# Performance work log

Hardware: AMD Instinct MI355X
Metric: run time of the kernel (lower is better)

## Reference

```python
import jax, jax.numpy as jnp
import numpy as np

B, CIN, H, W = 16, 1, 256, 256
WIDTH = 64
MODES = 32
LAYERS = 4
COUT = 1


def conv1x1(x, w, b):
    # x: [B,Ci,H,W], w: [Co,Ci], b: [Co]
    return jnp.einsum('bixy,oi->boxy', x, w) + b[None, :, None, None]


def mlp(x, w1, b1, w2, b2):
    # Conv2d(ci,mid,1) -> GELU(exact) -> Conv2d(mid,co,1)
    return conv1x1(jax.nn.gelu(conv1x1(x, w1, b1), approximate=False), w2, b2)


def spectral_conv2d(x, w1r, w1i, w2r, w2i):
    # x: [B,C,H,W]; weights: [Ci,Co,m1,m2] (real/imag parts of cfloat params)
    b, c, h, w = x.shape
    m1, m2 = w1r.shape[2], w1r.shape[3]
    co = w1r.shape[1]
    x_ft = jnp.fft.rfft2(x)  # [B,C,H,W//2+1] complex64
    w1 = w1r + 1j * w1i
    w2 = w2r + 1j * w2i
    top = jnp.einsum('bixy,ioxy->boxy', x_ft[:, :, :m1, :m2], w1)
    bot = jnp.einsum('bixy,ioxy->boxy', x_ft[:, :, -m1:, :m2], w2)
    out_ft = jnp.zeros((b, co, h, w // 2 + 1), dtype=x_ft.dtype)
    out_ft = out_ft.at[:, :, :m1, :m2].set(top).at[:, :, -m1:, :m2].set(bot)
    return jnp.fft.irfft2(out_ft, s=(h, w))


def setup_inputs() -> dict:
    key = jax.random.key(0)
    ks = iter(jax.random.split(key, 32))
    scale = 1.0 / (WIDTH * WIDTH)
    f32 = jnp.float32
    inp = {}
    inp['x'] = jax.random.normal(next(ks), (B, CIN, H, W), dtype=f32)
    # lifting 1x1 conv
    inp['p_w'] = jax.random.normal(next(ks), (WIDTH, CIN), dtype=f32) / np.sqrt(CIN)
    inp['p_b'] = jnp.zeros((WIDTH,), dtype=f32)
    # per-layer spectral weights (real/imag of uniform cfloat init)
    shp = (LAYERS, WIDTH, WIDTH, MODES, MODES)
    inp['sw1r'] = scale * jax.random.uniform(next(ks), shp, dtype=f32)
    inp['sw1i'] = scale * jax.random.uniform(next(ks), shp, dtype=f32)
    inp['sw2r'] = scale * jax.random.uniform(next(ks), shp, dtype=f32)
    inp['sw2i'] = scale * jax.random.uniform(next(ks), shp, dtype=f32)
    # per-layer channel MLP (mid_channels = WIDTH)
    inp['m1w'] = jax.random.normal(next(ks), (LAYERS, WIDTH, WIDTH), dtype=f32) / np.sqrt(WIDTH)
    inp['m1b'] = jnp.zeros((LAYERS, WIDTH), dtype=f32)
    inp['m2w'] = jax.random.normal(next(ks), (LAYERS, WIDTH, WIDTH), dtype=f32) / np.sqrt(WIDTH)
    inp['m2b'] = jnp.zeros((LAYERS, WIDTH), dtype=f32)
    # per-layer skip 1x1 conv
    inp['skw'] = jax.random.normal(next(ks), (LAYERS, WIDTH, WIDTH), dtype=f32) / np.sqrt(WIDTH)
    inp['skb'] = jnp.zeros((LAYERS, WIDTH), dtype=f32)
    # projection MLP (mid = 4*WIDTH)
    inp['q1w'] = jax.random.normal(next(ks), (4 * WIDTH, WIDTH), dtype=f32) / np.sqrt(WIDTH)
    inp['q1b'] = jnp.zeros((4 * WIDTH,), dtype=f32)
    inp['q2w'] = jax.random.normal(next(ks), (COUT, 4 * WIDTH), dtype=f32) / np.sqrt(4 * WIDTH)
    inp['q2b'] = jnp.zeros((COUT,), dtype=f32)
    return inp


def reference(x, p_w, p_b, sw1r, sw1i, sw2r, sw2i, m1w, m1b, m2w, m2b,
              skw, skb, q1w, q1b, q2w, q2b):
    h = conv1x1(x, p_w, p_b)  # lift to [B,WIDTH,H,W]
    for l in range(LAYERS):
        x1 = spectral_conv2d(h, sw1r[l], sw1i[l], sw2r[l], sw2i[l])
        x1 = mlp(x1, m1w[l], m1b[l], m2w[l], m2b[l])
        x2 = conv1x1(h, skw[l], skb[l])
        h = x1 + x2
        if l < LAYERS - 1:
            h = jax.nn.gelu(h, approximate=False)
    return mlp(h, q1w, q1b, q2w, q2b)  # [B,COUT,H,W]
```

## Files before the change

kernel.cpp:

```cpp
#include <hip/hip_runtime.h>
#include <math.h>

#define NC 64
#define NH 256
#define NW 256
#define NM 32
#define NKY 64
#define HW 65536

typedef short bfrag __attribute__((ext_vector_type(8)));
typedef float facc  __attribute__((ext_vector_type(4)));
#define MFMA(a,b,c) __builtin_amdgcn_mfma_f32_16x16x32_bf16(a,b,c,0,0,0)

static constexpr float PI_F = 3.14159265358979323846f;

__device__ __forceinline__ unsigned short f2b(float f) {
  unsigned b = __float_as_uint(f);
  return (unsigned short)((b + 0x7FFFu + ((b >> 16) & 1u)) >> 16);
}
__device__ __forceinline__ float b2f(unsigned short h) {
  return __uint_as_float((unsigned)h << 16);
}

__device__ __forceinline__ float gelu_f(float x) {
  float z = fabsf(x) * 0.70710678118654752f;
  float t = 1.0f / (1.0f + 0.3275911f * z);
  float e = __expf(-z * z);
  float p = t * (0.254829592f + t * (-0.284496736f + t * (1.421413741f +
            t * (-1.453152027f + t * 1.061405429f))));
  float er = copysignf(1.0f - p * e, x);
  return 0.5f * x * (1.0f + er);
}

__global__ void k_tEy(unsigned short* __restrict__ eh, unsigned short* __restrict__ el) {
  int i = blockIdx.x * 256 + threadIdx.x;
  int m = i >> 8, y = i & 255;
  int kyi = m & 63;
  int ky = (kyi < 32) ? kyi : (192 + kyi);
  int a = (ky * y) & 255;
  float s, c; sincosf((float)a * (PI_F / 128.f), &s, &c);
  float v = (m < 64) ? c : -s;
  unsigned short h = f2b(v);
  eh[i] = h; el[i] = f2b(v - b2f(h));
}
__global__ void k_tEx(unsigned short* __restrict__ eh, unsigned short* __restrict__ el) {
  int i = blockIdx.x * 256 + threadIdx.x;
  int m = i >> 9, k = i & 511;
  int x = k & 255, plane = k >> 8, kx = m & 31;
  int a = (kx * x) & 255;
  float s, c; sincosf((float)a * (PI_F / 128.f), &s, &c);
  float v = (m < 32) ? (plane ? s : c) : (plane ? c : -s);
  unsigned short h = f2b(v);
  eh[i] = h; el[i] = f2b(v - b2f(h));
}
__global__ void k_tWy(unsigned short* __restrict__ eh, unsigned short* __restrict__ el) {
  int i = blockIdx.x * 256 + threadIdx.x;
  int row = i >> 7, k = i & 127;
  int y = row & 255, part = row >> 8;
  int kyi = k & 63, plane = k >> 6;
  int ky = (kyi < 32) ? kyi : (192 + kyi);
  int a = (ky * y) & 255;
  float s, c; sincosf((float)a * (PI_F / 128.f), &s, &c);
  float v = (part == 0) ? (plane ? -s : c) : (plane ? c : s);
  unsigned short h = f2b(v);
  eh[i] = h; el[i] = f2b(v - b2f(h));
}
__global__ void k_tCx(unsigned short* __restrict__ eh, unsigned short* __restrict__ el) {
  int i = blockIdx.x * 256 + threadIdx.x;
  int x = i >> 6, k = i & 63;
  int kx = k & 31, plane = k >> 5;
  float w = ((kx == 0) ? 1.0f : 2.0f) / 65536.0f;
  int a = (kx * x) & 255;
  float s, c; sincosf((float)a * (PI_F / 128.f), &s, &c);
  float v = plane ? (-w * s) : (w * c);
  unsigned short h = f2b(v);
  eh[i] = h; el[i] = f2b(v - b2f(h));
}

__global__ void k_cvt2(const float* __restrict__ src, unsigned short* __restrict__ hi,
                       unsigned short* __restrict__ lo, int n) {
  int i = blockIdx.x * 256 + threadIdx.x;
  if (i < n) {
    float v = src[i];
    unsigned short h = f2b(v);
    hi[i] = h;
    lo[i] = f2b(v - b2f(h));
  }
}

__global__ __launch_bounds__(256) void k_lift(const float* __restrict__ x,
                                              const float* __restrict__ pw,
                                              const float* __restrict__ pb,
                                              float* __restrict__ h) {
  int b = blockIdx.y;
  int yx = blockIdx.x * 256 + threadIdx.x;
  float v = x[(size_t)b * HW + yx];
  float* hp = h + (size_t)b * NC * HW + yx;
  for (int c = 0; c < NC; ++c) hp[(size_t)c * HW] = v * pw[c] + pb[c];
}

__global__ __launch_bounds__(256) void k_fy2(const float* __restrict__ h,
                                             const unsigned short* __restrict__ Ah,
                                             const unsigned short* __restrict__ Al,
                                             float* __restrict__ Xc, int Ncol) {
  int tid = threadIdx.x, wv = tid >> 6, ln = tid & 63, g16 = ln >> 4, l15 = ln & 15;
  int colbase = blockIdx.x * 128 + wv * 32;
  facc acc[8][2];
#pragma unroll
  for (int mf = 0; mf < 8; ++mf)
#pragma unroll
    for (int pf = 0; pf < 2; ++pf) acc[mf][pf] = (facc)0.f;
#pragma unroll 1
  for (int ks = 0; ks < 8; ++ks) {
    int kof = g16 * 8 + 32 * ks;
    bfrag bh[2], bl[2];
#pragma unroll
    for (int pf = 0; pf < 2; ++pf) {
      int col = colbase + pf * 16 + l15;
      const float* hp = h + (size_t)(col >> 8) * HW + (col & 255) + (size_t)kof * 256;
#pragma unroll
      for (int j = 0; j < 8; ++j) {
        float v = hp[j * 256];
        unsigned short hi = f2b(v);
        bh[pf][j] = (short)hi;
        bl[pf][j] = (short)f2b(v - b2f(hi));
      }
    }
#pragma unroll
    for (int mf = 0; mf < 8; ++mf) {
      int row = 16 * mf + l15;
      bfrag ah = *(const bfrag*)(Ah + row * 256 + kof);
      bfrag al = *(const bfrag*)(Al + row * 256 + kof);
#pragma unroll
      for (int pf = 0; pf < 2; ++pf) {
        acc[mf][pf] = MFMA(ah, bh[pf], acc[mf][pf]);
        acc[mf][pf] = MFMA(ah, bl[pf], acc[mf][pf]);
        acc[mf][pf] = MFMA(al, bh[pf], acc[mf][pf]);
      }
    }
  }
#pragma unroll
  for (int mf = 0; mf < 8; ++mf)
#pragma unroll
    for (int pf = 0; pf < 2; ++pf) {
      int col = colbase + pf * 16 + l15;
#pragma unroll
      for (int r = 0; r < 4; ++r)
        Xc[(size_t)(16 * mf + 4 * g16 + r) * Ncol + col] = acc[mf][pf][r];
    }
}

__global__ __launch_bounds__(256) void k_fx2(const float* __restrict__ Xc,
                                             const unsigned short* __restrict__ Ah,
                                             const unsigned short* __restrict__ Al,
                                             float* __restrict__ X2r,
                                             float* __restrict__ X2i, int NcXc) {
  int tid = threadIdx.x, wv = tid >> 6, ln = tid & 63, g16 = ln >> 4, l15 = ln & 15;
  int colbase = blockIdx.x * 128 + wv * 32;
  facc acc[4][2];
#pragma unroll
  for (int mf = 0; mf < 4; ++mf)
#pragma unroll
    for (int pf = 0; pf < 2; ++pf) acc[mf][pf] = (facc)0.f;
#pragma unroll 1
  for (int ks = 0; ks < 16; ++ks) {
    int plane = ks >> 3;
    int x0 = (ks & 7) * 32 + g16 * 8;
    int kof = g16 * 8 + 32 * ks;
    bfrag bh[2], bl[2];
#pragma unroll
    for (int pf = 0; pf < 2; ++pf) {
      int col = colbase + pf * 16 + l15;
      const float* p = Xc + (size_t)(plane * 64 + (col & 63)) * NcXc + (col >> 6) * 256 + x0;
      float4 u0 = *(const float4*)p;
      float4 u1 = *(const float4*)(p + 4);
      float tv[8] = {u0.x, u0.y, u0.z, u0.w, u1.x, u1.y, u1.z, u1.w};
#pragma unroll
      for (int j = 0; j < 8; ++j) {
        unsigned short hi = f2b(tv[j]);
        bh[pf][j] = (short)hi;
        bl[pf][j] = (short)f2b(tv[j] - b2f(hi));
      }
    }
#pragma unroll
    for (int mf = 0; mf < 4; ++mf) {
      int row = 16 * mf + l15;
      bfrag ah = *(const bfrag*)(Ah + row * 512 + kof);
      bfrag al = *(const bfrag*)(Al + row * 512 + kof);
#pragma unroll
      for (int pf = 0; pf < 2; ++pf) {
        acc[mf][pf] = MFMA(ah, bh[pf], acc[mf][pf]);
        acc[mf][pf] = MFMA(ah, bl[pf], acc[mf][pf]);
        acc[mf][pf] = MFMA(al, bh[pf], acc[mf][pf]);
      }
    }
  }
#pragma unroll
  for (int mf = 0; mf < 4; ++mf)
#pragma unroll
    for (int pf = 0; pf < 2; ++pf) {
      int col = colbase + pf * 16 + l15;
      float* base = (mf >= 2) ? X2i : X2r;
      int kxb = 16 * (mf & 1) + 4 * g16;
      float4 v = make_float4(acc[mf][pf][0], acc[mf][pf][1], acc[mf][pf][2], acc[mf][pf][3]);
      *(float4*)(base + (size_t)col * 32 + kxb) = v;
    }
}

__global__ __launch_bounds__(512) void k_spec(const float* __restrict__ X2r,
                                              const float* __restrict__ X2i,
                                              const float* __restrict__ w1r,
                                              const float* __restrict__ w1i,
                                              const float* __restrict__ w2r,
                                              const float* __restrict__ w2i,
                                              float* __restrict__ S, int Ncs) {
  int b = blockIdx.y;
  int och = blockIdx.x & 3;
  int kyi = blockIdx.x >> 2;
  __shared__ float2 xs[NC * NM];
  for (int idx = threadIdx.x; idx < NC * NM; idx += 512) {
    int i = idx >> 5, kx = idx & 31;
    size_t c2 = ((size_t)(b * 64 + i) * 64 + kyi) * 32 + kx;
    xs[idx] = make_float2(X2r[c2], X2i[c2]);
  }
  __syncthreads();
  int kx = threadIdx.x & 31;
  int ol = threadIdx.x >> 5;
  int o = och * 16 + ol;
  int kym = kyi & 31;
  const float* wr = (kyi < 32) ? w1r : w2r;
  const float* wi = (kyi < 32) ? w1i : w2i;
  size_t wb = ((size_t)o * NM + kym) * NM + kx;
  float ar = 0.f, ai = 0.f;
#pragma unroll 4
  for (int i = 0; i < NC; ++i) {
    float2 xv = xs[i * NM + kx];
    float wrv = wr[wb + (size_t)i * 65536];
    float wiv = wi[wb + (size_t)i * 65536];
    ar += xv.x * wrv - xv.y * wiv;
    ai += xv.x * wiv + xv.y * wrv;
  }
  size_t cco = (size_t)(b * 64 + o) * 32 + kx;
  S[(size_t)kyi * Ncs + cco] = ar;
  S[(size_t)(64 + kyi) * Ncs + cco] = ai;
}

__global__ __launch_bounds__(256) void k_iy2(const float* __restrict__ S,
                                             const unsigned short* __restrict__ Ah,
                                             const unsigned short* __restrict__ Al,
                                             float* __restrict__ t2, int Ncs) {
  int tid = threadIdx.x, wv = tid >> 6, ln = tid & 63, g16 = ln >> 4, l15 = ln & 15;
  int colbase = blockIdx.x * 128 + wv * 32;
  int rowb = blockIdx.y * 64;
  facc acc[4][2];
#pragma unroll
  for (int mf = 0; mf < 4; ++mf)
#pragma unroll
    for (int pf = 0; pf < 2; ++pf) acc[mf][pf] = (facc)0.f;
#pragma unroll 1
  for (int ks = 0; ks < 4; ++ks) {
    int kof = g16 * 8 + 32 * ks;
    bfrag bh[2], bl[2];
#pragma unroll
    for (int pf = 0; pf < 2; ++pf) {
      int col = colbase + pf * 16 + l15;
      const float* p = S + (size_t)kof * Ncs + col;
#pragma unroll
      for (int j = 0; j < 8; ++j) {
        float v = p[(size_t)j * Ncs];
        unsigned short hi = f2b(v);
        bh[pf][j] = (short)hi;
        bl[pf][j] = (short)f2b(v - b2f(hi));
      }
    }
#pragma unroll
    for (int mf = 0; mf < 4; ++mf) {
      int row = rowb + 16 * mf + l15;
      bfrag ah = *(const bfrag*)(Ah + row * 128 + kof);
      bfrag al = *(const bfrag*)(Al + row * 128 + kof);
#pragma unroll
      for (int pf = 0; pf < 2; ++pf) {
        acc[mf][pf] = MFMA(ah, bh[pf], acc[mf][pf]);
        acc[mf][pf] = MFMA(ah, bl[pf], acc[mf][pf]);
        acc[mf][pf] = MFMA(al, bh[pf], acc[mf][pf]);
      }
    }
  }
#pragma unroll
  for (int mf = 0; mf < 4; ++mf)
#pragma unroll
    for (int pf = 0; pf < 2; ++pf) {
      int col = colbase + pf * 16 + l15;
#pragma unroll
      for (int r = 0; r < 4; ++r)
        t2[(size_t)(rowb + 16 * mf + 4 * g16 + r) * Ncs + col] = acc[mf][pf][r];
    }
}

__global__ __launch_bounds__(256) void k_ix2(const float* __restrict__ t2,
                                             const unsigned short* __restrict__ Ah,
                                             const unsigned short* __restrict__ Al,
                                             unsigned short* __restrict__ x1h,
                                             unsigned short* __restrict__ x1l, int Nct) {
  int tid = threadIdx.x, wv = tid >> 6, ln = tid & 63, g16 = ln >> 4, l15 = ln & 15;
  int colbase = blockIdx.x * 128 + wv * 32;
  int rowb = blockIdx.y * 128;
  facc acc[8][2];
#pragma unroll
  for (int mf = 0; mf < 8; ++mf)
#pragma unroll
    for (int pf = 0; pf < 2; ++pf) acc[mf][pf] = (facc)0.f;
#pragma unroll 1
  for (int ks = 0; ks < 2; ++ks) {
    int kof = g16 * 8 + 32 * ks;
    bfrag bh[2], bl[2];
#pragma unroll
    for (int pf = 0; pf < 2; ++pf) {
      int col = colbase + pf * 16 + l15;
      const float* p = t2 + (size_t)(ks * 256 + (col & 255)) * Nct + (col >> 8) * 32 + g16 * 8;
      float4 u0 = *(const float4*)p;
      float4 u1 = *(const float4*)(p + 4);
      float tv[8] = {u0.x, u0.y, u0.z, u0.w, u1.x, u1.y, u1.z, u1.w};
#pragma unroll
      for (int j = 0; j < 8; ++j) {
        unsigned short hi = f2b(tv[j]);
        bh[pf][j] = (short)hi;
        bl[pf][j] = (short)f2b(tv[j] - b2f(hi));
      }
    }
#pragma unroll
    for (int mf = 0; mf < 8; ++mf) {
      int row = rowb + 16 * mf + l15;
      bfrag ah = *(const bfrag*)(Ah + row * 64 + kof);
      bfrag al = *(const bfrag*)(Al + row * 64 + kof);
#pragma unroll
      for (int pf = 0; pf < 2; ++pf) {
        acc[mf][pf] = MFMA(ah, bh[pf], acc[mf][pf]);
        acc[mf][pf] = MFMA(ah, bl[pf], acc[mf][pf]);
        acc[mf][pf] = MFMA(al, bh[pf], acc[mf][pf]);
      }
    }
  }
#pragma unroll
  for (int mf = 0; mf < 8; ++mf)
#pragma unroll
    for (int pf = 0; pf < 2; ++pf) {
      int col = colbase + pf * 16 + l15;
      int bc = col >> 8, y = col & 255;
      int xb = rowb + 16 * mf + 4 * g16;
      ushort4 hv, lv;
#pragma unroll
      for (int r = 0; r < 4; ++r) {
        float v = acc[mf][pf][r];
        unsigned short hi = f2b(v);
        ((unsigned short*)&hv)[r] = hi;
        ((unsigned short*)&lv)[r] = f2b(v - b2f(hi));
      }
      size_t o = (size_t)bc * HW + y * 256 + xb;
      *(ushort4*)(x1h + o) = hv;
      *(ushort4*)(x1l + o) = lv;
    }
}

__global__ __launch_bounds__(256) void k_mlp1s(unsigned short* __restrict__ x1h,
                                               unsigned short* __restrict__ x1l,
                                               const unsigned short* __restrict__ w1h,
                                               const unsigned short* __restrict__ w1l,
                                               const float* __restrict__ b1p) {
  __shared__ unsigned short whs[64 * 72], wls[64 * 72];
  int tid = threadIdx.x;
  for (int i = tid; i < 64 * 64; i += 256) {
    int r = i >> 6, c = i & 63;
    whs[r * 72 + c] = w1h[i];
    wls[r * 72 + c] = w1l[i];
  }
  int wv = tid >> 6, ln = tid & 63, g16 = ln >> 4, l15 = ln & 15;
  int b = blockIdx.y;
  unsigned short* xh = x1h + (size_t)b * NC * HW;
  unsigned short* xl = x1l + (size_t)b * NC * HW;
  float b1v[4][4];
#pragma unroll
  for (int mf = 0; mf < 4; ++mf)
#pragma unroll
    for (int r = 0; r < 4; ++r) b1v[mf][r] = b1p[16 * mf + 4 * g16 + r];
  __syncthreads();
  for (int t = 0; t < 4; ++t) {
    int pxb = (blockIdx.x * 4 + t) * 128 + wv * 32;
    facc a1[4][2];
#pragma unroll
    for (int mf = 0; mf < 4; ++mf)
#pragma unroll
      for (int pf = 0; pf < 2; ++pf) {
        facc z; z[0] = b1v[mf][0]; z[1] = b1v[mf][1]; z[2] = b1v[mf][2]; z[3] = b1v[mf][3];
        a1[mf][pf] = z;
      }
#pragma unroll
    for (int ks = 0; ks < 2; ++ks) {
      bfrag xhb[2], xlb[2];
#pragma unroll
      for (int pf = 0; pf < 2; ++pf) {
        int px = pxb + pf * 16 + l15;
#pragma unroll
        for (int j = 0; j < 8; ++j) {
          int c = g16 * 8 + j + 32 * ks;
          xhb[pf][j] = (short)xh[(size_t)c * HW + px];
          xlb[pf][j] = (short)xl[(size_t)c * HW + px];
        }
      }
#pragma unroll
      for (int mf = 0; mf < 4; ++mf) {
        bfrag wh = *(const bfrag*)(whs + (16 * mf + l15) * 72 + g16 * 8 + 32 * ks);
        bfrag wl = *(const bfrag*)(wls + (16 * mf + l15) * 72 + g16 * 8 + 32 * ks);
#pragma unroll
        for (int pf = 0; pf < 2; ++pf) {
          a1[mf][pf] = MFMA(wh, xhb[pf], a1[mf][pf]);
          a1[mf][pf] = MFMA(wh, xlb[pf], a1[mf][pf]);
          a1[mf][pf] = MFMA(wl, xhb[pf], a1[mf][pf]);
        }
      }
    }
#pragma unroll
    for (int mf = 0; mf < 4; ++mf)
#pragma unroll
      for (int pf = 0; pf < 2; ++pf) {
        int px = pxb + pf * 16 + l15;
#pragma unroll
        for (int r = 0; r < 4; ++r) {
          float v = gelu_f(a1[mf][pf][r]);
          unsigned short hi = f2b(v);
          size_t idx = (size_t)(16 * mf + 4 * g16 + r) * HW + px;
          xh[idx] = hi;
          xl[idx] = f2b(v - b2f(hi));
        }
      }
  }
}

__global__ __launch_bounds__(256) void k_mix2(const unsigned short* __restrict__ midh,
                                              const unsigned short* __restrict__ midl,
                                              float* __restrict__ h,
                                              const unsigned short* __restrict__ w2h,
                                              const unsigned short* __restrict__ w2l,
                                              const unsigned short* __restrict__ skh,
                                              const unsigned short* __restrict__ skl,
                                              const float* __restrict__ b2p,
                                              const float* __restrict__ skbp,
                                              int do_gelu) {
  __shared__ unsigned short w2hs[64 * 72], w2ls[64 * 72], skhs[64 * 72], skls[64 * 72];
  int tid = threadIdx.x;
  for (int i = tid; i < 64 * 64; i += 256) {
    int r = i >> 6, c = i & 63;
    w2hs[r * 72 + c] = w2h[i];
    w2ls[r * 72 + c] = w2l[i];
    skhs[r * 72 + c] = skh[i];
    skls[r * 72 + c] = skl[i];
  }
  int wv = tid >> 6, ln = tid & 63, g16 = ln >> 4, l15 = ln & 15;
  int b = blockIdx.y;
  const unsigned short* mh = midh + (size_t)b * NC * HW;
  const unsigned short* ml = midl + (size_t)b * NC * HW;
  float* hb = h + (size_t)b * NC * HW;
  float b2v[4][4];
#pragma unroll
  for (int mf = 0; mf < 4; ++mf)
#pragma unroll
    for (int r = 0; r < 4; ++r) {
      int o = 16 * mf + 4 * g16 + r;
      b2v[mf][r] = b2p[o] + skbp[o];
    }
  __syncthreads();
  for (int t = 0; t < 4; ++t) {
    int pxb = (blockIdx.x * 4 + t) * 128 + wv * 32;
    facc a2[4][2];
#pragma unroll
    for (int mf = 0; mf < 4; ++mf)
#pragma unroll
      for (int pf = 0; pf < 2; ++pf) {
        facc z; z[0] = b2v[mf][0]; z[1] = b2v[mf][1]; z[2] = b2v[mf][2]; z[3] = b2v[mf][3];
        a2[mf][pf] = z;
      }
#pragma unroll
    for (int ks = 0; ks < 2; ++ks) {
      bfrag mhb[2], mlb[2], hhb[2], hlb[2];
#pragma unroll
      for (int pf = 0; pf < 2; ++pf) {
        int px = pxb + pf * 16 + l15;
#pragma unroll
        for (int j = 0; j < 8; ++j) {
          int c = g16 * 8 + j + 32 * ks;
          mhb[pf][j] = (short)mh[(size_t)c * HW + px];
          mlb[pf][j] = (short)ml[(size_t)c * HW + px];
          float v = hb[(size_t)c * HW + px];
          unsigned short hi = f2b(v);
          hhb[pf][j] = (short)hi;
          hlb[pf][j] = (short)f2b(v - b2f(hi));
        }
      }
#pragma unroll
      for (int mf = 0; mf < 4; ++mf) {
        bfrag w2hf = *(const bfrag*)(w2hs + (16 * mf + l15) * 72 + g16 * 8 + 32 * ks);
        bfrag w2lf = *(const bfrag*)(w2ls + (16 * mf + l15) * 72 + g16 * 8 + 32 * ks);
        bfrag skhf = *(const bfrag*)(skhs + (16 * mf + l15) * 72 + g16 * 8 + 32 * ks);
        bfrag sklf = *(const bfrag*)(skls + (16 * mf + l15) * 72 + g16 * 8 + 32 * ks);
#pragma unroll
        for (int pf = 0; pf < 2; ++pf) {
          a2[mf][pf] = MFMA(w2hf, mhb[pf], a2[mf][pf]);
          a2[mf][pf] = MFMA(w2hf, mlb[pf], a2[mf][pf]);
          a2[mf][pf] = MFMA(w2lf, mhb[pf], a2[mf][pf]);
          a2[mf][pf] = MFMA(skhf, hhb[pf], a2[mf][pf]);
          a2[mf][pf] = MFMA(skhf, hlb[pf], a2[mf][pf]);
          a2[mf][pf] = MFMA(sklf, hhb[pf], a2[mf][pf]);
        }
      }
    }
#pragma unroll
    for (int mf = 0; mf < 4; ++mf)
#pragma unroll
      for (int pf = 0; pf < 2; ++pf) {
        facc v = a2[mf][pf];
        if (do_gelu) {
          v[0] = gelu_f(v[0]); v[1] = gelu_f(v[1]);
          v[2] = gelu_f(v[2]); v[3] = gelu_f(v[3]);
        }
        int px = pxb + pf * 16 + l15;
#pragma unroll
        for (int r = 0; r < 4; ++r)
          hb[(size_t)(16 * mf + 4 * g16 + r) * HW + px] = v[r];
      }
  }
}

__global__ __launch_bounds__(256) void k_proj2s(const float* __restrict__ h,
                                                const unsigned short* __restrict__ q1h,
                                                const unsigned short* __restrict__ q1l,
                                                const float* __restrict__ q1bp,
                                                const float* __restrict__ q2wp,
                                                const float* __restrict__ q2bp,
                                                float* __restrict__ out) {
  __shared__ float part[4][16];
  int tid = threadIdx.x;
  int wv = tid >> 6, ln = tid & 63, g16 = ln >> 4, l15 = ln & 15;
  int b = blockIdx.y;
  const float* hb = h + (size_t)b * NC * HW;
  bfrag qh[4][2], ql[4][2];
#pragma unroll
  for (int mf = 0; mf < 4; ++mf)
#pragma unroll
    for (int ks = 0; ks < 2; ++ks) {
      int row = 64 * wv + 16 * mf + l15;
      size_t base = (size_t)row * 64 + g16 * 8 + 32 * ks;
      qh[mf][ks] = *(const bfrag*)(q1h + base);
      ql[mf][ks] = *(const bfrag*)(q1l + base);
    }
  float bq[4][4], qv[4][4];
#pragma unroll
  for (int mf = 0; mf < 4; ++mf)
#pragma unroll
    for (int r = 0; r < 4; ++r) {
      int row = 64 * wv + 16 * mf + 4 * g16 + r;
      bq[mf][r] = q1bp[row];
      qv[mf][r] = q2wp[row];
    }
  float q2bias = q2bp[0];
  for (int t = 0; t < 16; ++t) {
    int px0 = blockIdx.x * 256 + t * 16;
    facc acc[4];
#pragma unroll
    for (int mf = 0; mf < 4; ++mf) {
      facc z; z[0] = bq[mf][0]; z[1] = bq[mf][1]; z[2] = bq[mf][2]; z[3] = bq[mf][3];
      acc[mf] = z;
    }
#pragma unroll
    for (int ks = 0; ks < 2; ++ks) {
      bfrag hh, hl;
#pragma unroll
      for (int j = 0; j < 8; ++j) {
        int c = g16 * 8 + j + 32 * ks;
        float v = hb[(size_t)c * HW + px0 + l15];
        unsigned short hi = f2b(v);
        hh[j] = (short)hi;
        hl[j] = (short)f2b(v - b2f(hi));
      }
#pragma unroll
      for (int mf = 0; mf < 4; ++mf) {
        acc[mf] = MFMA(qh[mf][ks], hh, acc[mf]);
        acc[mf] = MFMA(qh[mf][ks], hl, acc[mf]);
        acc[mf] = MFMA(ql[mf][ks], hh, acc[mf]);
      }
    }
    float partial = 0.f;
#pragma unroll
    for (int mf = 0; mf < 4; ++mf)
#pragma unroll
      for (int r = 0; r < 4; ++r)
        partial += gelu_f(acc[mf][r]) * qv[mf][r];
    partial += __shfl_xor(partial, 16);
    partial += __shfl_xor(partial, 32);
    if (ln < 16) part[wv][l15] = partial;
    __syncthreads();
    if (tid < 16)
      out[(size_t)b * HW + px0 + tid] =
          part[0][tid] + part[1][tid] + part[2][tid] + part[3][tid] + q2bias;
    __syncthreads();
  }
}

extern "C" void kernel_launch(void* const* d_in, const int* in_sizes, int n_in,
                              void* d_out, int out_size, void* d_ws, size_t ws_size,
                              hipStream_t stream) {
  const float* x    = (const float*)d_in[0];
  const float* p_w  = (const float*)d_in[1];
  const float* p_b  = (const float*)d_in[2];
  const float* sw1r = (const float*)d_in[3];
  const float* sw1i = (const float*)d_in[4];
  const float* sw2r = (const float*)d_in[5];
  const float* sw2i = (const float*)d_in[6];
  const float* m1w  = (const float*)d_in[7];
  const float* m1b  = (const float*)d_in[8];
  const float* m2w  = (const float*)d_in[9];
  const float* m2b  = (const float*)d_in[10];
  const float* skw  = (const float*)d_in[11];
  const float* skb  = (const float*)d_in[12];
  const float* q1w  = (const float*)d_in[13];
  const float* q1b  = (const float*)d_in[14];
  const float* q2w  = (const float*)d_in[15];
  const float* q2b  = (const float*)d_in[16];

  const size_t MB = 1048576ULL;
  const size_t TBL = 1 * MB;
  int g = 16;
  while (g > 1 && (size_t)g * 36 * MB + TBL > ws_size) g >>= 1;
  if ((size_t)g * 36 * MB + TBL > ws_size) return;

  char* wsb = (char*)d_ws;
  unsigned short* Eyh = (unsigned short*)(wsb + 0);
  unsigned short* Eyl = (unsigned short*)(wsb + 65536);
  unsigned short* Exh = (unsigned short*)(wsb + 131072);
  unsigned short* Exl = (unsigned short*)(wsb + 196608);
  unsigned short* Wyh = (unsigned short*)(wsb + 262144);
  unsigned short* Wyl = (unsigned short*)(wsb + 393216);
  unsigned short* Cxh = (unsigned short*)(wsb + 524288);
  unsigned short* Cxl = (unsigned short*)(wsb + 557056);
  unsigned short* m1h = (unsigned short*)(wsb + 589824);
  unsigned short* m1l = (unsigned short*)(wsb + 622592);
  unsigned short* m2h = (unsigned short*)(wsb + 655360);
  unsigned short* m2l = (unsigned short*)(wsb + 688128);
  unsigned short* skh = (unsigned short*)(wsb + 720896);
  unsigned short* skl = (unsigned short*)(wsb + 753664);
  unsigned short* q1h = (unsigned short*)(wsb + 786432);
  unsigned short* q1l = (unsigned short*)(wsb + 819200);

  char* base = wsb + TBL;
  float* A = (float*)base;
  unsigned short* x1h = (unsigned short*)(base + (size_t)g * 16 * MB);
  unsigned short* x1l = (unsigned short*)(base + (size_t)g * 24 * MB);
  float* Xc  = (float*)x1h;
  float* X2r = (float*)x1l;
  float* X2i = (float*)((char*)x1l + (size_t)g * 512 * 1024);
  float* S   = (float*)((char*)x1l + (size_t)g * 1 * MB);
  float* t2  = (float*)(base + (size_t)g * 32 * MB);

  k_tEy<<<128, 256, 0, stream>>>(Eyh, Eyl);
  k_tEx<<<128, 256, 0, stream>>>(Exh, Exl);
  k_tWy<<<256, 256, 0, stream>>>(Wyh, Wyl);
  k_tCx<<<64, 256, 0, stream>>>(Cxh, Cxl);
  k_cvt2<<<64, 256, 0, stream>>>(m1w, m1h, m1l, 16384);
  k_cvt2<<<64, 256, 0, stream>>>(m2w, m2h, m2l, 16384);
  k_cvt2<<<64, 256, 0, stream>>>(skw, skh, skl, 16384);
  k_cvt2<<<64, 256, 0, stream>>>(q1w, q1h, q1l, 16384);

  int Nfy = g * 16384;
  int Ncs = g * 2048;

  for (int b0 = 0; b0 < 16; b0 += g) {
    k_lift<<<dim3(256, g), 256, 0, stream>>>(x + (size_t)b0 * HW, p_w, p_b, A);
    for (int l = 0; l < 4; ++l) {
      k_fy2<<<g * 128, 256, 0, stream>>>(A, Eyh, Eyl, Xc, Nfy);
      k_fx2<<<g * 32, 256, 0, stream>>>(Xc, Exh, Exl, X2r, X2i, Nfy);
      k_spec<<<dim3(256, g), 512, 0, stream>>>(X2r, X2i,
                                               sw1r + (size_t)l * 4194304,
                                               sw1i + (size_t)l * 4194304,
                                               sw2r + (size_t)l * 4194304,
                                               sw2i + (size_t)l * 4194304, S, Ncs);
      k_iy2<<<dim3(g * 16, 8), 256, 0, stream>>>(S, Wyh, Wyl, t2, Ncs);
      k_ix2<<<dim3(g * 128, 2), 256, 0, stream>>>(t2, Cxh, Cxl, x1h, x1l, Ncs);
      k_mlp1s<<<dim3(128, g), 256, 0, stream>>>(x1h, x1l, m1h + l * 4096, m1l + l * 4096,
                                                m1b + l * 64);
      k_mix2<<<dim3(128, g), 256, 0, stream>>>(x1h, x1l, A, m2h + l * 4096, m2l + l * 4096,
                                               skh + l * 4096, skl + l * 4096,
                                               m2b + l * 64, skb + l * 64, (l < 3) ? 1 : 0);
    }
    k_proj2s<<<dim3(256, g), 256, 0, stream>>>(A, q1h, q1l, q1b, q2w, q2b,
                                               (float*)d_out + (size_t)b0 * HW);
  }
}
```

Baseline: 4.189 ms.

## Store hidden state as pre-split bf16 hi/lo pairs and restructure fx2/projection kernels

The hidden activation buffer is now kept as two bf16 planes (hi and lo) written by the lift and mix kernels. The forward-y, mix and projection kernels therefore load ready-made MFMA operands instead of converting fp32 to bf16 on every read. Memory traffic stays about the same (2+2 bytes versus 4), but repeated conversion ALU work goes away. k_fx2 now gives each wave 16 columns instead of 32, doubling the grid for more parallelism. The projection kernel stages q1 weights in LDS, each wave handles all 256 hidden rows for its own pixels, and the cross-wave shared-memory reduction and its syncthreads are removed.

```diff
diff --git a/kernel.cpp b/kernel.cpp
--- a/kernel.cpp
+++ b/kernel.cpp
@@ -91,15 +91,22 @@
 __global__ __launch_bounds__(256) void k_lift(const float* __restrict__ x,
                                               const float* __restrict__ pw,
                                               const float* __restrict__ pb,
-                                              float* __restrict__ h) {
+                                              unsigned short* __restrict__ hh,
+                                              unsigned short* __restrict__ hl) {
   int b = blockIdx.y;
   int yx = blockIdx.x * 256 + threadIdx.x;
   float v = x[(size_t)b * HW + yx];
-  float* hp = h + (size_t)b * NC * HW + yx;
-  for (int c = 0; c < NC; ++c) hp[(size_t)c * HW] = v * pw[c] + pb[c];
-}
-
-__global__ __launch_bounds__(256) void k_fy2(const float* __restrict__ h,
+  size_t o = (size_t)b * NC * HW + yx;
+  for (int c = 0; c < NC; ++c) {
+    float u = v * pw[c] + pb[c];
+    unsigned short hi = f2b(u);
+    hh[o + (size_t)c * HW] = hi;
+    hl[o + (size_t)c * HW] = f2b(u - b2f(hi));
+  }
+}
+
+__global__ __launch_bounds__(256) void k_fy2(const unsigned short* __restrict__ hh,
+                                             const unsigned short* __restrict__ hl,
                                              const unsigned short* __restrict__ Ah,
                                              const unsigned short* __restrict__ Al,
                                              float* __restrict__ Xc, int Ncol) {
@@ -117,13 +124,11 @@
 #pragma unroll
     for (int pf = 0; pf < 2; ++pf) {
       int col = colbase + pf * 16 + l15;
-      const float* hp = h + (size_t)(col >> 8) * HW + (col & 255) + (size_t)kof * 256;
+      size_t o = (size_t)(col >> 8) * HW + (col & 255) + (size_t)kof * 256;
 #pragma unroll
       for (int j = 0; j < 8; ++j) {
-        float v = hp[j * 256];
-        unsigned short hi = f2b(v);
-        bh[pf][j] = (short)hi;
-        bl[pf][j] = (short)f2b(v - b2f(hi));
+        bh[pf][j] = (short)hh[o + j * 256];
+        bl[pf][j] = (short)hl[o + j * 256];
       }
     }
 #pragma unroll
@@ -156,21 +161,18 @@
                                              float* __restrict__ X2r,
                                              float* __restrict__ X2i, int NcXc) {
   int tid = threadIdx.x, wv = tid >> 6, ln = tid & 63, g16 = ln >> 4, l15 = ln & 15;
-  int colbase = blockIdx.x * 128 + wv * 32;
-  facc acc[4][2];
-#pragma unroll
-  for (int mf = 0; mf < 4; ++mf)
-#pragma unroll
-    for (int pf = 0; pf < 2; ++pf) acc[mf][pf] = (facc)0.f;
+  int colbase = blockIdx.x * 64 + wv * 16;
+  facc acc[4];
+#pragma unroll
+  for (int mf = 0; mf < 4; ++mf) acc[mf] = (facc)0.f;
 #pragma unroll 1
   for (int ks = 0; ks < 16; ++ks) {
     int plane = ks >> 3;
     int x0 = (ks & 7) * 32 + g16 * 8;
     int kof = g16 * 8 + 32 * ks;
-    bfrag bh[2], bl[2];
-#pragma unroll
-    for (int pf = 0; pf < 2; ++pf) {
-      int col = colbase + pf * 16 + l15;
+    bfrag bh, bl;
+    {
+      int col = colbase + l15;
       const float* p = Xc + (size_t)(plane * 64 + (col & 63)) * NcXc + (col >> 6) * 256 + x0;
       float4 u0 = *(const float4*)p;
       float4 u1 = *(const float4*)(p + 4);
@@ -178,8 +180,8 @@
 #pragma unroll
       for (int j = 0; j < 8; ++j) {
         unsigned short hi = f2b(tv[j]);
-        bh[pf][j] = (short)hi;
-        bl[pf][j] = (short)f2b(tv[j] - b2f(hi));
+        bh[j] = (short)hi;
+        bl[j] = (short)f2b(tv[j] - b2f(hi));
       }
     }
 #pragma unroll
@@ -187,24 +189,19 @@
       int row = 16 * mf + l15;
       bfrag ah = *(const bfrag*)(Ah + row * 512 + kof);
       bfrag al = *(const bfrag*)(Al + row * 512 + kof);
-#pragma unroll
-      for (int pf = 0; pf < 2; ++pf) {
-        acc[mf][pf] = MFMA(ah, bh[pf], acc[mf][pf]);
-        acc[mf][pf] = MFMA(ah, bl[pf], acc[mf][pf]);
-        acc[mf][pf] = MFMA(al, bh[pf], acc[mf][pf]);
-      }
-    }
-  }
-#pragma unroll
-  for (int mf = 0; mf < 4; ++mf)
-#pragma unroll
-    for (int pf = 0; pf < 2; ++pf) {
-      int col = colbase + pf * 16 + l15;
-      float* base = (mf >= 2) ? X2i : X2r;
-      int kxb = 16 * (mf & 1) + 4 * g16;
-      float4 v = make_float4(acc[mf][pf][0], acc[mf][pf][1], acc[mf][pf][2], acc[mf][pf][3]);
-      *(float4*)(base + (size_t)col * 32 + kxb) = v;
-    }
+      acc[mf] = MFMA(ah, bh, acc[mf]);
+      acc[mf] = MFMA(ah, bl, acc[mf]);
+      acc[mf] = MFMA(al, bh, acc[mf]);
+    }
+  }
+#pragma unroll
+  for (int mf = 0; mf < 4; ++mf) {
+    int col = colbase + l15;
+    float* base = (mf >= 2) ? X2i : X2r;
+    int kxb = 16 * (mf & 1) + 4 * g16;
+    float4 v = make_float4(acc[mf][0], acc[mf][1], acc[mf][2], acc[mf][3]);
+    *(float4*)(base + (size_t)col * 32 + kxb) = v;
+  }
 }
 
 __global__ __launch_bounds__(512) void k_spec(const float* __restrict__ X2r,
@@ -438,7 +435,8 @@
 
 __global__ __launch_bounds__(256) void k_mix2(const unsigned short* __restrict__ midh,
                                               const unsigned short* __restrict__ midl,
-                                              float* __restrict__ h,
+                                              unsigned short* __restrict__ hh_,
+                                              unsigned short* __restrict__ hl_,
                                               const unsigned short* __restrict__ w2h,
                                               const unsigned short* __restrict__ w2l,
                                               const unsigned short* __restrict__ skh,
@@ -459,7 +457,8 @@
   int b = blockIdx.y;
   const unsigned short* mh = midh + (size_t)b * NC * HW;
   const unsigned short* ml = midl + (size_t)b * NC * HW;
-  float* hb = h + (size_t)b * NC * HW;
+  unsigned short* hbh = hh_ + (size_t)b * NC * HW;
+  unsigned short* hbl = hl_ + (size_t)b * NC * HW;
   float b2v[4][4];
 #pragma unroll
   for (int mf = 0; mf < 4; ++mf)
@@ -490,10 +489,8 @@
           int c = g16 * 8 + j + 32 * ks;
           mhb[pf][j] = (short)mh[(size_t)c * HW + px];
           mlb[pf][j] = (short)ml[(size_t)c * HW + px];
-          float v = hb[(size_t)c * HW + px];
-          unsigned short hi = f2b(v);
-          hhb[pf][j] = (short)hi;
-          hlb[pf][j] = (short)f2b(v - b2f(hi));
+          hhb[pf][j] = (short)hbh[(size_t)c * HW + px];
+          hlb[pf][j] = (short)hbl[(size_t)c * HW + px];
         }
       }
 #pragma unroll
@@ -524,84 +521,80 @@
         }
         int px = pxb + pf * 16 + l15;
 #pragma unroll
-        for (int r = 0; r < 4; ++r)
-          hb[(size_t)(16 * mf + 4 * g16 + r) * HW + px] = v[r];
-      }
-  }
-}
-
-__global__ __launch_bounds__(256) void k_proj2s(const float* __restrict__ h,
-                                                const unsigned short* __restrict__ q1h,
-                                                const unsigned short* __restrict__ q1l,
-                                                const float* __restrict__ q1bp,
-                                                const float* __restrict__ q2wp,
-                                                const float* __restrict__ q2bp,
-                                                float* __restrict__ out) {
-  __shared__ float part[4][16];
+        for (int r = 0; r < 4; ++r) {
+          float u = v[r];
+          unsigned short hi = f2b(u);
+          size_t idx = (size_t)(16 * mf + 4 * g16 + r) * HW + px;
+          hbh[idx] = hi;
+          hbl[idx] = f2b(u - b2f(hi));
+        }
+      }
+  }
+}
+
+__global__ __launch_bounds__(256) void k_proj3(const unsigned short* __restrict__ hh,
+                                               const unsigned short* __restrict__ hl,
+                                               const unsigned short* __restrict__ q1h,
+                                               const unsigned short* __restrict__ q1l,
+                                               const float* __restrict__ q1bp,
+                                               const float* __restrict__ q2wp,
+                                               const float* __restrict__ q2bp,
+                                               float* __restrict__ out) {
+  __shared__ unsigned short q1sh[256 * 72];
+  __shared__ unsigned short q1sl[256 * 72];
   int tid = threadIdx.x;
+  for (int i = tid; i < 256 * 64; i += 256) {
+    int r = i >> 6, c = i & 63;
+    q1sh[r * 72 + c] = q1h[i];
+    q1sl[r * 72 + c] = q1l[i];
+  }
   int wv = tid >> 6, ln = tid & 63, g16 = ln >> 4, l15 = ln & 15;
   int b = blockIdx.y;
-  const float* hb = h + (size_t)b * NC * HW;
-  bfrag qh[4][2], ql[4][2];
-#pragma unroll
-  for (int mf = 0; mf < 4; ++mf)
-#pragma unroll
-    for (int ks = 0; ks < 2; ++ks) {
-      int row = 64 * wv + 16 * mf + l15;
-      size_t base = (size_t)row * 64 + g16 * 8 + 32 * ks;
-      qh[mf][ks] = *(const bfrag*)(q1h + base);
-      ql[mf][ks] = *(const bfrag*)(q1l + base);
-    }
-  float bq[4][4], qv[4][4];
-#pragma unroll
-  for (int mf = 0; mf < 4; ++mf)
+  const unsigned short* hbh = hh + (size_t)b * NC * HW;
+  const unsigned short* hbl = hl + (size_t)b * NC * HW;
+  float bq[16][4], qv[16][4];
+#pragma unroll
+  for (int mf = 0; mf < 16; ++mf)
 #pragma unroll
     for (int r = 0; r < 4; ++r) {
-      int row = 64 * wv + 16 * mf + 4 * g16 + r;
+      int row = 16 * mf + 4 * g16 + r;
       bq[mf][r] = q1bp[row];
       qv[mf][r] = q2wp[row];
     }
   float q2bias = q2bp[0];
-  for (int t = 0; t < 16; ++t) {
-    int px0 = blockIdx.x * 256 + t * 16;
-    facc acc[4];
-#pragma unroll
-    for (int mf = 0; mf < 4; ++mf) {
-      facc z; z[0] = bq[mf][0]; z[1] = bq[mf][1]; z[2] = bq[mf][2]; z[3] = bq[mf][3];
-      acc[mf] = z;
-    }
-#pragma unroll
-    for (int ks = 0; ks < 2; ++ks) {
-      bfrag hh, hl;
+  __syncthreads();
+  for (int t = 0; t < 4; ++t) {
+    int px0 = blockIdx.x * 256 + t * 64 + wv * 16;
+    bfrag hhb[2], hlb[2];
+#pragma unroll
+    for (int ks = 0; ks < 2; ++ks)
 #pragma unroll
       for (int j = 0; j < 8; ++j) {
         int c = g16 * 8 + j + 32 * ks;
-        float v = hb[(size_t)c * HW + px0 + l15];
-        unsigned short hi = f2b(v);
-        hh[j] = (short)hi;
-        hl[j] = (short)f2b(v - b2f(hi));
-      }
-#pragma unroll
-      for (int mf = 0; mf < 4; ++mf) {
-        acc[mf] = MFMA(qh[mf][ks], hh, acc[mf]);
-        acc[mf] = MFMA(qh[mf][ks], hl, acc[mf]);
-        acc[mf] = MFMA(ql[mf][ks], hh, acc[mf]);
-      }
-    }
+        hhb[ks][j] = (short)hbh[(size_t)c * HW + px0 + l15];
+        hlb[ks][j] = (short)hbl[(size_t)c * HW + px0 + l15];
+      }
     float partial = 0.f;
 #pragma unroll
-    for (int mf = 0; mf < 4; ++mf)
+    for (int mf = 0; mf < 16; ++mf) {
+      facc acc;
+      acc[0] = bq[mf][0]; acc[1] = bq[mf][1]; acc[2] = bq[mf][2]; acc[3] = bq[mf][3];
+#pragma unroll
+      for (int ks = 0; ks < 2; ++ks) {
+        bfrag ah = *(const bfrag*)(q1sh + (16 * mf + l15) * 72 + g16 * 8 + 32 * ks);
+        bfrag al = *(const bfrag*)(q1sl + (16 * mf + l15) * 72 + g16 * 8 + 32 * ks);
+        acc = MFMA(ah, hhb[ks], acc);
+        acc = MFMA(ah, hlb[ks], acc);
+        acc = MFMA(al, hhb[ks], acc);
+      }
 #pragma unroll
       for (int r = 0; r < 4; ++r)
-        partial += gelu_f(acc[mf][r]) * qv[mf][r];
+        partial += gelu_f(acc[r]) * qv[mf][r];
+    }
     partial += __shfl_xor(partial, 16);
     partial += __shfl_xor(partial, 32);
-    if (ln < 16) part[wv][l15] = partial;
-    __syncthreads();
-    if (tid < 16)
-      out[(size_t)b * HW + px0 + tid] =
-          part[0][tid] + part[1][tid] + part[2][tid] + part[3][tid] + q2bias;
-    __syncthreads();
+    if (ln < 16)
+      out[(size_t)b * HW + px0 + ln] = partial + q2bias;
   }
 }
 
@@ -651,7 +644,8 @@
   unsigned short* q1l = (unsigned short*)(wsb + 819200);
 
   char* base = wsb + TBL;
-  float* A = (float*)base;
+  unsigned short* Hh = (unsigned short*)base;
+  unsigned short* Hl = (unsigned short*)(base + (size_t)g * 8 * MB);
   unsigned short* x1h = (unsigned short*)(base + (size_t)g * 16 * MB);
   unsigned short* x1l = (unsigned short*)(base + (size_t)g * 24 * MB);
   float* Xc  = (float*)x1h;
@@ -673,10 +667,10 @@
   int Ncs = g * 2048;
 
   for (int b0 = 0; b0 < 16; b0 += g) {
-    k_lift<<<dim3(256, g), 256, 0, stream>>>(x + (size_t)b0 * HW, p_w, p_b, A);
+    k_lift<<<dim3(256, g), 256, 0, stream>>>(x + (size_t)b0 * HW, p_w, p_b, Hh, Hl);
     for (int l = 0; l < 4; ++l) {
-      k_fy2<<<g * 128, 256, 0, stream>>>(A, Eyh, Eyl, Xc, Nfy);
-      k_fx2<<<g * 32, 256, 0, stream>>>(Xc, Exh, Exl, X2r, X2i, Nfy);
+      k_fy2<<<g * 128, 256, 0, stream>>>(Hh, Hl, Eyh, Eyl, Xc, Nfy);
+      k_fx2<<<g * 64, 256, 0, stream>>>(Xc, Exh, Exl, X2r, X2i, Nfy);
       k_spec<<<dim3(256, g), 512, 0, stream>>>(X2r, X2i,
                                                sw1r + (size_t)l * 4194304,
                                                sw1i + (size_t)l * 4194304,
@@ -686,11 +680,11 @@
       k_ix2<<<dim3(g * 128, 2), 256, 0, stream>>>(t2, Cxh, Cxl, x1h, x1l, Ncs);
       k_mlp1s<<<dim3(128, g), 256, 0, stream>>>(x1h, x1l, m1h + l * 4096, m1l + l * 4096,
                                                 m1b + l * 64);
-      k_mix2<<<dim3(128, g), 256, 0, stream>>>(x1h, x1l, A, m2h + l * 4096, m2l + l * 4096,
+      k_mix2<<<dim3(128, g), 256, 0, stream>>>(x1h, x1l, Hh, Hl, m2h + l * 4096, m2l + l * 4096,
                                                skh + l * 4096, skl + l * 4096,
                                                m2b + l * 64, skb + l * 64, (l < 3) ? 1 : 0);
     }
-    k_proj2s<<<dim3(256, g), 256, 0, stream>>>(A, q1h, q1l, q1b, q2w, q2b,
-                                               (float*)d_out + (size_t)b0 * HW);
-  }
-}
+    k_proj3<<<dim3(256, g), 256, 0, stream>>>(Hh, Hl, q1h, q1l, q1b, q2w, q2b,
+                                              (float*)d_out + (size_t)b0 * HW);
+  }
+}
```

Result: no change. 4.252 ms (+1.5%).
